# Kernel tuning notes

Hardware: AMD Instinct MI355X
Metric: run time of the kernel (lower is better)

Reference implementation:

```python
import jax, jax.numpy as jnp
import numpy as np

B, S, F, H = 256, 512, 64, 128


def setup_inputs() -> dict:
    key = jax.random.key(0)
    ks = jax.random.split(key, 16)
    u = lambda k, shape, fan: jax.random.uniform(k, shape, jnp.float32, -1.0 / np.sqrt(fan), 1.0 / np.sqrt(fan))
    inp = {
        'x': jax.random.normal(ks[0], (B, S, F), jnp.float32),
        'm': (jax.random.uniform(ks[1], (B, S, F)) < 0.8).astype(jnp.float32),
        't': jax.random.uniform(ks[2], (B, S, F), jnp.float32),
        # temp_decay_h: Linear(F -> H)
        'Wdh': u(ks[3], (H, F), H), 'bdh': u(ks[4], (H,), H),
        # temp_decay_m: diagonal Linear(F -> F)
        'Wdm': u(ks[5], (F, F), F), 'bdm': u(ks[6], (F,), F),
        # time_reg: Linear(H -> F)
        'Wtr': u(ks[7], (F, H), H), 'btr': u(ks[8], (F,), H),
        # feat_reg: masked Linear(F -> F), zero diagonal
        'Wfr': u(ks[9], (F, F), F), 'bfr': u(ks[10], (F,), F),
        # weight_combine: Linear(2F -> F)
        'Wwc': u(ks[11], (F, 2 * F), 2 * F), 'bwc': u(ks[12], (F,), 2 * F),
        # LSTMCell(2F -> H)
        'Wih': u(ks[13], (4 * H, 2 * F), H), 'Whh': u(ks[14], (4 * H, H), H),
        'bih': u(ks[15], (4 * H,), H), 'bhh': u(jax.random.fold_in(key, 99), (4 * H,), H),
    }
    return inp


def _rits_forward(x, m, t, Wdh, bdh, Wdm, bdm, Wtr, btr, Wfr, bfr, Wwc, bwc, Wih, Whh, bih, bhh):
    f = x.shape[-1]
    hdim = Whh.shape[1]
    dWdm = jnp.diagonal(Wdm)                 # diag-masked temporal decay weight
    Wfr_m = Wfr * (1.0 - jnp.eye(f, dtype=Wfr.dtype))

    def step(carry, inputs):
        h, c, loss = carry
        xl, ml, tl = inputs                  # [B,F] each
        gamma_h = jnp.exp(-jax.nn.relu(tl @ Wdh.T + bdh))   # [B,H]
        gamma_m = jnp.exp(-jax.nn.relu(tl * dWdm + bdm))    # [B,F]
        h = h * gamma_h
        xl_hat = h @ Wtr.T + btr             # history-based estimate [B,F]
        denom = jnp.sum(ml) + 1e-5
        loss = loss + jnp.sum((xl - xl_hat) ** 2 * ml) / denom
        xl_c = ml * xl + (1.0 - ml) * xl_hat
        zl_hat = xl_c @ Wfr_m.T + bfr        # feature-based estimate
        loss = loss + jnp.sum((xl - zl_hat) ** 2 * ml) / denom
        beta = jnp.concatenate([gamma_m, ml], axis=1) @ Wwc.T + bwc
        cl_hat = beta * zl_hat + (1.0 - beta) * xl_hat
        loss = loss + jnp.sum((xl - cl_hat) ** 2 * ml) / denom
        cl_c = ml * xl + (1.0 - ml) * cl_hat
        inp = jnp.concatenate([cl_c, ml], axis=1)           # [B,2F]
        gates = inp @ Wih.T + bih + h @ Whh.T + bhh         # [B,4H]
        i, fg, g, o = jnp.split(gates, 4, axis=1)
        i, fg, o = jax.nn.sigmoid(i), jax.nn.sigmoid(fg), jax.nn.sigmoid(o)
        c = fg * c + i * jnp.tanh(g)
        h = o * jnp.tanh(c)
        return (h, c, loss), cl_c

    b, s, _ = x.shape
    h0 = jnp.zeros((b, hdim), x.dtype)
    c0 = jnp.zeros((b, hdim), x.dtype)
    xs = (jnp.swapaxes(x, 0, 1), jnp.swapaxes(m, 0, 1), jnp.swapaxes(t, 0, 1))
    (h, c, loss), imps = jax.lax.scan(step, (h0, c0, jnp.float32(0.0)), xs)
    imputations = jnp.swapaxes(imps, 0, 1)   # [B,S,F]
    return imputations, loss / s


def reference(x, m, t, Wdh, bdh, Wdm, bdm, Wtr, btr, Wfr, bfr, Wwc, bwc, Wih, Whh, bih, bhh):
    return _rits_forward(x, m, t, Wdh, bdh, Wdm, bdm, Wtr, btr, Wfr, bfr, Wwc, bwc, Wih, Whh, bih, bhh)
```

## Files before the change

kernel.cpp:

```cpp
#include <hip/hip_runtime.h>
#include <hip/hip_bf16.h>

#define Bsz 256
#define Ssz 512
#define Fsz 64
#define Hsz 128
#define NG  512

typedef unsigned short ushort_t;
typedef __attribute__((ext_vector_type(8))) short short8v;
typedef __attribute__((ext_vector_type(4))) float float4v;

__device__ __forceinline__ ushort_t f2bf(float f) {
  unsigned int b = __float_as_uint(f);
  return (ushort_t)((b + 0x7fffu + ((b >> 16) & 1u)) >> 16);
}
__device__ __forceinline__ float bf2f(ushort_t u) {
  return __uint_as_float(((unsigned int)u) << 16);
}
__device__ __forceinline__ float sigf(float v) { return 1.f / (1.f + __expf(-v)); }
__device__ __forceinline__ float tanhf_fast(float v) {
  float e = __expf(2.f * v);
  return 1.f - 2.f / (e + 1.f);
}

__global__ void denom_kernel(const float* __restrict__ m, float* __restrict__ inv_denom) {
  int s = blockIdx.x;
  int tid = threadIdx.x;
  const float4* mp = (const float4*)(m + ((size_t)tid * Ssz + s) * Fsz);
  float sum = 0.f;
#pragma unroll
  for (int i = 0; i < Fsz / 4; ++i) {
    float4 v = mp[i];
    sum += v.x + v.y + v.z + v.w;
  }
  for (int off = 32; off > 0; off >>= 1) sum += __shfl_xor(sum, off);
  __shared__ float red[4];
  if ((tid & 63) == 0) red[tid >> 6] = sum;
  __syncthreads();
  if (tid == 0) {
    float tot = red[0] + red[1] + red[2] + red[3];
    inv_denom[s] = 1.0f / (tot + 1e-5f);
  }
}

__global__ void pack_kernel(const float* __restrict__ Wih, const float* __restrict__ Whh,
                            ushort_t* __restrict__ Wpk) {
  int g = blockIdx.x * blockDim.x + threadIdx.x;
  if (g >= 16384) return;
  int lane = g & 63, nt = (g >> 6) & 31, kt = g >> 11;
  int jout = nt * 16 + (lane & 15);
  int kbase = kt * 32 + ((lane >> 4) << 3);
  ushort_t* dst = Wpk + (size_t)g * 8;
#pragma unroll
  for (int j = 0; j < 8; ++j) {
    int k = kbase + j;
    float w = (k < 128) ? Wih[jout * 128 + k] : Whh[jout * 128 + (k - 128)];
    dst[j] = f2bf(w);
  }
}

__global__ void gh_kernel(const float* __restrict__ t, const float* __restrict__ Wdh,
                          const float* __restrict__ bdh, ushort_t* __restrict__ gh) {
  const int tid = threadIdx.x;
  const int lane = tid & 63, wv = tid >> 6;
  const int row0 = blockIdx.x * 64;
  __shared__ __align__(16) ushort_t st[64][72];
  __shared__ __align__(16) ushort_t sO[64][136];
  __shared__ float sbdh[128];
  if (tid < 128) sbdh[tid] = bdh[tid];
  short8v Bf[2][8];
#pragma unroll
  for (int kt = 0; kt < 2; ++kt)
#pragma unroll
    for (int nt = 0; nt < 8; ++nt) {
      int col = nt * 16 + (lane & 15);
      int k0 = kt * 32 + ((lane >> 4) << 3);
      float4 wa = *(const float4*)(Wdh + col * 64 + k0);
      float4 wb = *(const float4*)(Wdh + col * 64 + k0 + 4);
      short8v bb;
      bb[0] = (short)f2bf(wa.x); bb[1] = (short)f2bf(wa.y);
      bb[2] = (short)f2bf(wa.z); bb[3] = (short)f2bf(wa.w);
      bb[4] = (short)f2bf(wb.x); bb[5] = (short)f2bf(wb.y);
      bb[6] = (short)f2bf(wb.z); bb[7] = (short)f2bf(wb.w);
      Bf[kt][nt] = bb;
    }
  const float* tb = t + (size_t)row0 * 64;
  {
    int r = tid >> 2, c0 = (tid & 3) * 16;
#pragma unroll
    for (int q = 0; q < 4; ++q) {
      float4 v = *(const float4*)(tb + r * 64 + c0 + q * 4);
      st[r][c0 + q * 4 + 0] = f2bf(v.x);
      st[r][c0 + q * 4 + 1] = f2bf(v.y);
      st[r][c0 + q * 4 + 2] = f2bf(v.z);
      st[r][c0 + q * 4 + 3] = f2bf(v.w);
    }
  }
  __syncthreads();
  float4v acc[8] = {};
#pragma unroll
  for (int kt = 0; kt < 2; ++kt) {
    int r = wv * 16 + (lane & 15);
    int k0 = kt * 32 + ((lane >> 4) << 3);
    short8v a = *(const short8v*)&st[r][k0];
#pragma unroll
    for (int nt = 0; nt < 8; ++nt)
      acc[nt] = __builtin_amdgcn_mfma_f32_16x16x32_bf16(a, Bf[kt][nt], acc[nt], 0, 0, 0);
  }
#pragma unroll
  for (int nt = 0; nt < 8; ++nt)
#pragma unroll
    for (int rr = 0; rr < 4; ++rr) {
      int col = nt * 16 + (lane & 15);
      int row = wv * 16 + ((lane >> 4) << 2) + rr;
      float v = acc[nt][rr] + sbdh[col];
      sO[row][col] = f2bf(__expf(-fmaxf(0.f, v)));
    }
  __syncthreads();
  {
    int r = tid >> 2, c0 = (tid & 3) * 32;
    const uint4* src = (const uint4*)&sO[r][c0];
    uint4* dst = (uint4*)(gh + (size_t)(row0 + r) * 128 + c0);
#pragma unroll
    for (int q = 0; q < 4; ++q) dst[q] = src[q];
  }
}

__global__ void beta_kernel(const float* __restrict__ t, const float* __restrict__ m,
                            const float* __restrict__ Wdm, const float* __restrict__ bdm,
                            const float* __restrict__ Wwc, const float* __restrict__ bwc,
                            ushort_t* __restrict__ beta) {
  const int tid = threadIdx.x;
  const int lane = tid & 63, wv = tid >> 6;
  const int row0 = blockIdx.x * 64;
  __shared__ __align__(16) ushort_t sA[64][136];
  __shared__ __align__(16) ushort_t sO[64][72];
  __shared__ float sdw[64], sbd[64], sbwc[64];
  if (tid < 64) {
    sdw[tid] = Wdm[tid * 64 + tid];
    sbd[tid] = bdm[tid];
    sbwc[tid] = bwc[tid];
  }
  short8v Bf[4][4];
#pragma unroll
  for (int kt = 0; kt < 4; ++kt)
#pragma unroll
    for (int nt = 0; nt < 4; ++nt) {
      int col = nt * 16 + (lane & 15);
      int k0 = kt * 32 + ((lane >> 4) << 3);
      float4 wa = *(const float4*)(Wwc + col * 128 + k0);
      float4 wb = *(const float4*)(Wwc + col * 128 + k0 + 4);
      short8v bb;
      bb[0] = (short)f2bf(wa.x); bb[1] = (short)f2bf(wa.y);
      bb[2] = (short)f2bf(wa.z); bb[3] = (short)f2bf(wa.w);
      bb[4] = (short)f2bf(wb.x); bb[5] = (short)f2bf(wb.y);
      bb[6] = (short)f2bf(wb.z); bb[7] = (short)f2bf(wb.w);
      Bf[kt][nt] = bb;
    }
  __syncthreads();
  {
    int r = tid >> 2, c0 = (tid & 3) * 16;
    const float* tb = t + (size_t)row0 * 64;
    const float* mb = m + (size_t)row0 * 64;
#pragma unroll
    for (int q = 0; q < 4; ++q) {
      float4 tv = *(const float4*)(tb + r * 64 + c0 + q * 4);
      float4 mv = *(const float4*)(mb + r * 64 + c0 + q * 4);
      int c = c0 + q * 4;
      sA[r][c + 0] = f2bf(__expf(-fmaxf(0.f, tv.x * sdw[c + 0] + sbd[c + 0])));
      sA[r][c + 1] = f2bf(__expf(-fmaxf(0.f, tv.y * sdw[c + 1] + sbd[c + 1])));
      sA[r][c + 2] = f2bf(__expf(-fmaxf(0.f, tv.z * sdw[c + 2] + sbd[c + 2])));
      sA[r][c + 3] = f2bf(__expf(-fmaxf(0.f, tv.w * sdw[c + 3] + sbd[c + 3])));
      sA[r][64 + c + 0] = f2bf(mv.x);
      sA[r][64 + c + 1] = f2bf(mv.y);
      sA[r][64 + c + 2] = f2bf(mv.z);
      sA[r][64 + c + 3] = f2bf(mv.w);
    }
  }
  __syncthreads();
  float4v acc[4] = {};
#pragma unroll
  for (int kt = 0; kt < 4; ++kt) {
    int r = wv * 16 + (lane & 15);
    int k0 = kt * 32 + ((lane >> 4) << 3);
    short8v a = *(const short8v*)&sA[r][k0];
#pragma unroll
    for (int nt = 0; nt < 4; ++nt)
      acc[nt] = __builtin_amdgcn_mfma_f32_16x16x32_bf16(a, Bf[kt][nt], acc[nt], 0, 0, 0);
  }
#pragma unroll
  for (int nt = 0; nt < 4; ++nt)
#pragma unroll
    for (int rr = 0; rr < 4; ++rr) {
      int col = nt * 16 + (lane & 15);
      int row = wv * 16 + ((lane >> 4) << 2) + rr;
      sO[row][col] = f2bf(acc[nt][rr] + sbwc[col]);
    }
  __syncthreads();
  {
    int r = tid >> 2, c0 = (tid & 3) * 16;
    const uint4* src = (const uint4*)&sO[r][c0];
    uint4* dst = (uint4*)(beta + (size_t)(row0 + r) * 64 + c0);
    dst[0] = src[0];
    dst[1] = src[1];
  }
}

__launch_bounds__(512, 1)
__global__ void rits_kernel(
    const float* __restrict__ x, const float* __restrict__ m,
    const float* __restrict__ Wtr, const float* __restrict__ btr,
    const float* __restrict__ Wfr, const float* __restrict__ bfr,
    const float* __restrict__ bih, const float* __restrict__ bhh,
    const ushort_t* __restrict__ Wpk, const float* __restrict__ inv_denom,
    const ushort_t* __restrict__ ghp, const ushort_t* __restrict__ betap,
    float* __restrict__ out_imp, float* __restrict__ out_loss)
{
  const int b = blockIdx.x;
  const int tid = threadIdx.x;
  const int lane = tid & 63;
  const int wv = tid >> 6;

  __shared__ float sIdn[Ssz];
  __shared__ float sPart[8][64];
  __shared__ float sPartF[8][64];
  __shared__ float sGates[NG];
  __shared__ float sH[Hsz];
  __shared__ __align__(16) ushort_t sVh[256];

  sIdn[tid] = inv_denom[tid];

  float wtr_r[16];
  {
    const float* wb = Wtr + lane * 128 + wv * 16;
#pragma unroll
    for (int q = 0; q < 4; ++q) {
      float4 v = *(const float4*)(wb + q * 4);
      wtr_r[q * 4 + 0] = v.x; wtr_r[q * 4 + 1] = v.y;
      wtr_r[q * 4 + 2] = v.z; wtr_r[q * 4 + 3] = v.w;
    }
  }
  float wfr_r[8];
  {
    const float* wb = Wfr + lane * 64 + wv * 8;
#pragma unroll
    for (int q = 0; q < 2; ++q) {
      float4 v = *(const float4*)(wb + q * 4);
      wfr_r[q * 4 + 0] = v.x; wfr_r[q * 4 + 1] = v.y;
      wfr_r[q * 4 + 2] = v.z; wfr_r[q * 4 + 3] = v.w;
    }
#pragma unroll
    for (int i = 0; i < 8; ++i)
      if (lane == wv * 8 + i) wfr_r[i] = 0.f;
  }
  const float btr_r = btr[lane];
  const float bfr_r = bfr[lane];

  const short8v* wp = (const short8v*)Wpk;
  short8v Bf[8][4];
#pragma unroll
  for (int kt = 0; kt < 8; ++kt)
#pragma unroll
    for (int n = 0; n < 4; ++n)
      Bf[kt][n] = wp[((kt * 32 + wv * 4 + n) << 6) + lane];
  float gb[4];
#pragma unroll
  for (int n = 0; n < 4; ++n) {
    int j = (wv * 4 + n) * 16 + (lane & 15);
    gb[n] = bih[j] + bhh[j];
  }

  const float* xp = x + (size_t)b * Ssz * Fsz;
  const float* mp = m + (size_t)b * Ssz * Fsz;
  const ushort_t* ghb = ghp + (size_t)b * Ssz * 128;
  const ushort_t* beb = betap + (size_t)b * Ssz * 64;
  float* op = out_imp + (size_t)b * Ssz * Fsz;

  if (tid < Hsz) sH[tid] = 0.f;
  if (tid < 128) sVh[128 + tid] = 0;
  float c_reg = 0.f;

  float xv_cur = xp[lane];
  float mv_cur = mp[lane];
  float bet_cur = bf2f(beb[lane]);
  if (wv == 0) sVh[64 + lane] = f2bf(mv_cur);
  __syncthreads();

  float lacc = 0.f;

  for (int s = 0; s < Ssz; ++s) {
    const int ps = (s + 1 < Ssz) ? s + 1 : Ssz - 1;
    float xv_nxt = xp[ps * 64 + lane];
    float mv_nxt = mp[ps * 64 + lane];
    ushort_t bet_raw = beb[ps * 64 + lane];
    ushort_t gh_raw = 0;
    if (tid < 128) gh_raw = ghb[(size_t)ps * 128 + tid];

    {
      const float4* h4 = (const float4*)&sH[wv * 16];
      float4 h0 = h4[0], h1 = h4[1], h2 = h4[2], h3 = h4[3];
      float part = wtr_r[0] * h0.x + wtr_r[1] * h0.y + wtr_r[2] * h0.z + wtr_r[3] * h0.w
                 + wtr_r[4] * h1.x + wtr_r[5] * h1.y + wtr_r[6] * h1.z + wtr_r[7] * h1.w
                 + wtr_r[8] * h2.x + wtr_r[9] * h2.y + wtr_r[10] * h2.z + wtr_r[11] * h2.w
                 + wtr_r[12] * h3.x + wtr_r[13] * h3.y + wtr_r[14] * h3.z + wtr_r[15] * h3.w;
      sPart[wv][lane] = part;
    }

    float4v acc[4];
#pragma unroll
    for (int n = 0; n < 4; ++n) acc[n] = (float4v){gb[n], gb[n], gb[n], gb[n]};
    {
      const char* abase = (const char*)sVh + ((lane >> 4) << 4);
#pragma unroll
      for (int kt = 2; kt < 8; ++kt) {
        short8v a = *(const short8v*)(abase + kt * 64);
#pragma unroll
        for (int n = 0; n < 4; ++n)
          acc[n] = __builtin_amdgcn_mfma_f32_16x16x32_bf16(a, Bf[kt][n], acc[n], 0, 0, 0);
      }
    }
    __syncthreads();

    float xlh = btr_r;
#pragma unroll
    for (int w = 0; w < 8; ++w) xlh += sPart[w][lane];
    const float xv = xv_cur, mv = mv_cur;
    const float xlc = mv * xv + (1.f - mv) * xlh;
    const float idn = sIdn[s];
    if (wv == 0) { float d = xv - xlh; lacc += d * d * mv * idn; }
    {
      float pf = 0.f;
#pragma unroll
      for (int i = 0; i < 8; ++i) pf += wfr_r[i] * __shfl(xlc, wv * 8 + i);
      sPartF[wv][lane] = pf;
    }
    __syncthreads();

    float zl = bfr_r;
#pragma unroll
    for (int w = 0; w < 8; ++w) zl += sPartF[w][lane];
    const float beta = bet_cur;
    const float clh = beta * zl + (1.f - beta) * xlh;
    const float clc = mv * xv + (1.f - mv) * clh;
    if (wv == 0) {
      float d2 = xv - zl, d3 = xv - clh;
      lacc += (d2 * d2 + d3 * d3) * mv * idn;
      op[s * 64 + lane] = clc;
    }
    {
      const int kb = (lane >> 4) << 3;
      short8v A0, A1;
#pragma unroll
      for (int j = 0; j < 8; ++j) {
        A0[j] = (short)f2bf(__shfl(clc, kb + j));
        A1[j] = (short)f2bf(__shfl(clc, 32 + kb + j));
      }
#pragma unroll
      for (int n = 0; n < 4; ++n) {
        acc[n] = __builtin_amdgcn_mfma_f32_16x16x32_bf16(A0, Bf[0][n], acc[n], 0, 0, 0);
        acc[n] = __builtin_amdgcn_mfma_f32_16x16x32_bf16(A1, Bf[1][n], acc[n], 0, 0, 0);
      }
      if (lane < 16) {
#pragma unroll
        for (int n = 0; n < 4; ++n)
          sGates[(wv * 4 + n) * 16 + lane] = acc[n][0];
      }
    }
    __syncthreads();

    if (tid < 128) {
      float gi = sGates[tid], gf = sGates[128 + tid];
      float gg = sGates[256 + tid], go = sGates[384 + tid];
      float cc = sigf(gf) * c_reg + sigf(gi) * tanhf_fast(gg);
      c_reg = cc;
      float hn = sigf(go) * tanhf_fast(cc);
      float hv = hn * bf2f(gh_raw);
      sH[tid] = hv;
      sVh[128 + tid] = f2bf(hv);
    }
    if (wv == 0) sVh[64 + lane] = f2bf(mv_nxt);
    __syncthreads();

    xv_cur = xv_nxt;
    mv_cur = mv_nxt;
    bet_cur = bf2f(bet_raw);
  }

  if (wv == 0) {
    for (int off = 32; off > 0; off >>= 1) lacc += __shfl_xor(lacc, off);
    if (lane == 0) atomicAdd(out_loss, lacc * (1.0f / Ssz));
  }
}

extern "C" void kernel_launch(void* const* d_in, const int* in_sizes, int n_in,
                              void* d_out, int out_size, void* d_ws, size_t ws_size,
                              hipStream_t stream) {
  const float* x   = (const float*)d_in[0];
  const float* m   = (const float*)d_in[1];
  const float* t   = (const float*)d_in[2];
  const float* Wdh = (const float*)d_in[3];
  const float* bdh = (const float*)d_in[4];
  const float* Wdm = (const float*)d_in[5];
  const float* bdm = (const float*)d_in[6];
  const float* Wtr = (const float*)d_in[7];
  const float* btr = (const float*)d_in[8];
  const float* Wfr = (const float*)d_in[9];
  const float* bfr = (const float*)d_in[10];
  const float* Wwc = (const float*)d_in[11];
  const float* bwc = (const float*)d_in[12];
  const float* Wih = (const float*)d_in[13];
  const float* Whh = (const float*)d_in[14];
  const float* bih = (const float*)d_in[15];
  const float* bhh = (const float*)d_in[16];

  char* ws = (char*)d_ws;
  float* inv_denom = (float*)ws;
  ushort_t* Wpk    = (ushort_t*)(ws + 2048);
  ushort_t* gh_ws  = (ushort_t*)(ws + 264192);
  ushort_t* be_ws  = (ushort_t*)(ws + 264192 + (size_t)Bsz * Ssz * 128 * 2);
  float* out_f = (float*)d_out;
  float* out_loss = out_f + (size_t)Bsz * Ssz * Fsz;

  denom_kernel<<<Ssz, 256, 0, stream>>>(m, inv_denom);
  pack_kernel<<<64, 256, 0, stream>>>(Wih, Whh, Wpk);
  gh_kernel<<<(Bsz * Ssz) / 64, 256, 0, stream>>>(t, Wdh, bdh, gh_ws);
  beta_kernel<<<(Bsz * Ssz) / 64, 256, 0, stream>>>(t, m, Wdm, bdm, Wwc, bwc, be_ws);
  hipMemsetAsync(out_loss, 0, sizeof(float), stream);
  rits_kernel<<<Bsz, 512, 0, stream>>>(x, m, Wtr, btr, Wfr, bfr, bih, bhh,
                                       Wpk, inv_denom, gh_ws, be_ws, out_f, out_loss);
}
```

Baseline: 1.486 ms.

## Restructure RITS recurrence with MFMA regressions, gate-local LSTM, chunked staging

The history regression (Wtr) and feature regression (Wfr) move from per-lane fp32 dot products plus shared-memory partial reductions onto bf16 MFMA tiles held by a few waves. Gate columns are reassigned so each wave holds the i/f/g/o tiles for the same 16 hidden units, so the LSTM update runs in registers without a shared gates buffer. This cuts the per-step barriers from four to three. Per-step global loads of x, m, beta and gamma_h are replaced by 8-step double-buffered chunks staged into LDS. The regressions now take bf16 inputs, which loses precision, and the feature-regression stage runs on a single wave that sits on the critical path.

```diff
diff --git a/kernel.cpp b/kernel.cpp
--- a/kernel.cpp
+++ b/kernel.cpp
@@ -6,6 +6,7 @@
 #define Fsz 64
 #define Hsz 128
 #define NG  512
+#define CH  8
 
 typedef unsigned short ushort_t;
 typedef __attribute__((ext_vector_type(8))) short short8v;
@@ -22,6 +23,11 @@
 __device__ __forceinline__ float tanhf_fast(float v) {
   float e = __expf(2.f * v);
   return 1.f - 2.f / (e + 1.f);
+}
+__device__ __forceinline__ void bar_sync() {
+  asm volatile("s_waitcnt lgkmcnt(0)" ::: "memory");
+  __builtin_amdgcn_s_barrier();
+  asm volatile("" ::: "memory");
 }
 
 __global__ void denom_kernel(const float* __restrict__ m, float* __restrict__ inv_denom) {
@@ -221,41 +227,21 @@
   const int tid = threadIdx.x;
   const int lane = tid & 63;
   const int wv = tid >> 6;
+  const int l15 = lane & 15;
+  const int kg = lane >> 4;
 
   __shared__ float sIdn[Ssz];
-  __shared__ float sPart[8][64];
-  __shared__ float sPartF[8][64];
-  __shared__ float sGates[NG];
-  __shared__ float sH[Hsz];
-  __shared__ __align__(16) ushort_t sVh[256];
+  __shared__ __align__(16) ushort_t sHh[Hsz];
+  __shared__ __align__(16) ushort_t sXcF[Fsz];
+  __shared__ __align__(16) ushort_t sClcF[Fsz];
+  __shared__ float sXlhP[2][Fsz];
+  __shared__ __align__(16) float    sXb[2][CH][Fsz];
+  __shared__ __align__(16) ushort_t sMb[2][CH][Fsz];
+  __shared__ __align__(16) ushort_t sBb[2][CH][Fsz];
+  __shared__ __align__(16) ushort_t sGb[2][CH][Hsz];
 
   sIdn[tid] = inv_denom[tid];
-
-  float wtr_r[16];
-  {
-    const float* wb = Wtr + lane * 128 + wv * 16;
-#pragma unroll
-    for (int q = 0; q < 4; ++q) {
-      float4 v = *(const float4*)(wb + q * 4);
-      wtr_r[q * 4 + 0] = v.x; wtr_r[q * 4 + 1] = v.y;
-      wtr_r[q * 4 + 2] = v.z; wtr_r[q * 4 + 3] = v.w;
-    }
-  }
-  float wfr_r[8];
-  {
-    const float* wb = Wfr + lane * 64 + wv * 8;
-#pragma unroll
-    for (int q = 0; q < 2; ++q) {
-      float4 v = *(const float4*)(wb + q * 4);
-      wfr_r[q * 4 + 0] = v.x; wfr_r[q * 4 + 1] = v.y;
-      wfr_r[q * 4 + 2] = v.z; wfr_r[q * 4 + 3] = v.w;
-    }
-#pragma unroll
-    for (int i = 0; i < 8; ++i)
-      if (lane == wv * 8 + i) wfr_r[i] = 0.f;
-  }
-  const float btr_r = btr[lane];
-  const float bfr_r = bfr[lane];
+  if (tid < Hsz) sHh[tid] = 0;
 
   const short8v* wp = (const short8v*)Wpk;
   short8v Bf[8][4];
@@ -263,132 +249,210 @@
   for (int kt = 0; kt < 8; ++kt)
 #pragma unroll
     for (int n = 0; n < 4; ++n)
-      Bf[kt][n] = wp[((kt * 32 + wv * 4 + n) << 6) + lane];
+      Bf[kt][n] = wp[((kt * 32 + wv + 8 * n) << 6) + lane];
   float gb[4];
 #pragma unroll
   for (int n = 0; n < 4; ++n) {
-    int j = (wv * 4 + n) * 16 + (lane & 15);
+    int j = (wv + 8 * n) * 16 + l15;
     gb[n] = bih[j] + bhh[j];
+  }
+
+  short8v uW[8];
+  float btr_r[4] = {0.f, 0.f, 0.f, 0.f}, bfr_r[4] = {0.f, 0.f, 0.f, 0.f};
+  if (wv == 1 || wv == 3) {
+    const int ktb = (wv == 1) ? 0 : 2;
+#pragma unroll
+    for (int kt = 0; kt < 2; ++kt)
+#pragma unroll
+      for (int n = 0; n < 4; ++n) {
+        int col = n * 16 + l15;
+        int k0 = (ktb + kt) * 32 + kg * 8;
+        short8v bb;
+#pragma unroll
+        for (int j = 0; j < 8; ++j) bb[j] = (short)f2bf(Wtr[col * 128 + k0 + j]);
+        uW[kt * 4 + n] = bb;
+      }
+  } else if (wv == 2) {
+#pragma unroll
+    for (int kt = 0; kt < 2; ++kt)
+#pragma unroll
+      for (int n = 0; n < 4; ++n) {
+        int col = n * 16 + l15;
+        int k0 = kt * 32 + kg * 8;
+        short8v bb;
+#pragma unroll
+        for (int j = 0; j < 8; ++j) {
+          int k = k0 + j;
+          bb[j] = (k == col) ? (short)0 : (short)f2bf(Wfr[col * 64 + k]);
+        }
+        uW[kt * 4 + n] = bb;
+      }
+#pragma unroll
+    for (int n = 0; n < 4; ++n) {
+      btr_r[n] = btr[n * 16 + l15];
+      bfr_r[n] = bfr[n * 16 + l15];
+    }
   }
 
   const float* xp = x + (size_t)b * Ssz * Fsz;
   const float* mp = m + (size_t)b * Ssz * Fsz;
-  const ushort_t* ghb = ghp + (size_t)b * Ssz * 128;
-  const ushort_t* beb = betap + (size_t)b * Ssz * 64;
+  const ushort_t* ghb = ghp + (size_t)b * Ssz * Hsz;
+  const ushort_t* beb = betap + (size_t)b * Ssz * Fsz;
   float* op = out_imp + (size_t)b * Ssz * Fsz;
 
-  if (tid < Hsz) sH[tid] = 0.f;
-  if (tid < 128) sVh[128 + tid] = 0;
+  {
+    float x0 = xp[tid], m0 = mp[tid];
+    ushort_t b0 = beb[tid];
+    int st0 = 1 + (tid >> 7);
+    int st1 = st0 + 4;
+    ushort_t g0 = ghb[(size_t)st0 * Hsz + (tid & 127)];
+    ushort_t g1 = ghb[(size_t)st1 * Hsz + (tid & 127)];
+    sXb[0][tid >> 6][tid & 63] = x0;
+    sMb[0][tid >> 6][tid & 63] = f2bf(m0);
+    sBb[0][tid >> 6][tid & 63] = b0;
+    sGb[0][tid >> 7][tid & 127] = g0;
+    sGb[0][4 + (tid >> 7)][tid & 127] = g1;
+  }
+  __syncthreads();
+
+  float lacc = 0.f;
   float c_reg = 0.f;
-
-  float xv_cur = xp[lane];
-  float mv_cur = mp[lane];
-  float bet_cur = bf2f(beb[lane]);
-  if (wv == 0) sVh[64 + lane] = f2bf(mv_cur);
-  __syncthreads();
-
-  float lacc = 0.f;
+  float x_r = 0.f, m_r = 0.f;
+  ushort_t be_r = 0, gh_r0 = 0, gh_r1 = 0;
 
   for (int s = 0; s < Ssz; ++s) {
-    const int ps = (s + 1 < Ssz) ? s + 1 : Ssz - 1;
-    float xv_nxt = xp[ps * 64 + lane];
-    float mv_nxt = mp[ps * 64 + lane];
-    ushort_t bet_raw = beb[ps * 64 + lane];
-    ushort_t gh_raw = 0;
-    if (tid < 128) gh_raw = ghb[(size_t)ps * 128 + tid];
-
-    {
-      const float4* h4 = (const float4*)&sH[wv * 16];
-      float4 h0 = h4[0], h1 = h4[1], h2 = h4[2], h3 = h4[3];
-      float part = wtr_r[0] * h0.x + wtr_r[1] * h0.y + wtr_r[2] * h0.z + wtr_r[3] * h0.w
-                 + wtr_r[4] * h1.x + wtr_r[5] * h1.y + wtr_r[6] * h1.z + wtr_r[7] * h1.w
-                 + wtr_r[8] * h2.x + wtr_r[9] * h2.y + wtr_r[10] * h2.z + wtr_r[11] * h2.w
-                 + wtr_r[12] * h3.x + wtr_r[13] * h3.y + wtr_r[14] * h3.z + wtr_r[15] * h3.w;
-      sPart[wv][lane] = part;
-    }
+    const int p = (s >> 3) & 1, sc = s & 7;
+
+    if (sc == 0 && s + CH < Ssz) {
+      int base = (s + CH) * Fsz;
+      x_r = xp[base + tid];
+      m_r = mp[base + tid];
+      be_r = beb[base + tid];
+      int st0 = s + CH + 1 + (tid >> 7);
+      int st1 = st0 + 4;
+      if (st0 > Ssz - 1) st0 = Ssz - 1;
+      if (st1 > Ssz - 1) st1 = Ssz - 1;
+      gh_r0 = ghb[(size_t)st0 * Hsz + (tid & 127)];
+      gh_r1 = ghb[(size_t)st1 * Hsz + (tid & 127)];
+    }
+    const char* hbase = (const char*)sHh + kg * 16;
+    short8v ah0 = *(const short8v*)(hbase);
+    short8v ah1 = *(const short8v*)(hbase + 64);
+    short8v ah2 = *(const short8v*)(hbase + 128);
+    short8v ah3 = *(const short8v*)(hbase + 192);
+    const char* mbase = (const char*)sMb[p][sc] + kg * 16;
+    short8v am0 = *(const short8v*)(mbase);
+    short8v am1 = *(const short8v*)(mbase + 64);
 
     float4v acc[4];
 #pragma unroll
     for (int n = 0; n < 4; ++n) acc[n] = (float4v){gb[n], gb[n], gb[n], gb[n]};
-    {
-      const char* abase = (const char*)sVh + ((lane >> 4) << 4);
-#pragma unroll
-      for (int kt = 2; kt < 8; ++kt) {
-        short8v a = *(const short8v*)(abase + kt * 64);
-#pragma unroll
-        for (int n = 0; n < 4; ++n)
-          acc[n] = __builtin_amdgcn_mfma_f32_16x16x32_bf16(a, Bf[kt][n], acc[n], 0, 0, 0);
-      }
-    }
-    __syncthreads();
-
-    float xlh = btr_r;
-#pragma unroll
-    for (int w = 0; w < 8; ++w) xlh += sPart[w][lane];
-    const float xv = xv_cur, mv = mv_cur;
-    const float xlc = mv * xv + (1.f - mv) * xlh;
-    const float idn = sIdn[s];
-    if (wv == 0) { float d = xv - xlh; lacc += d * d * mv * idn; }
-    {
-      float pf = 0.f;
-#pragma unroll
-      for (int i = 0; i < 8; ++i) pf += wfr_r[i] * __shfl(xlc, wv * 8 + i);
-      sPartF[wv][lane] = pf;
-    }
-    __syncthreads();
-
-    float zl = bfr_r;
-#pragma unroll
-    for (int w = 0; w < 8; ++w) zl += sPartF[w][lane];
-    const float beta = bet_cur;
-    const float clh = beta * zl + (1.f - beta) * xlh;
-    const float clc = mv * xv + (1.f - mv) * clh;
-    if (wv == 0) {
-      float d2 = xv - zl, d3 = xv - clh;
-      lacc += (d2 * d2 + d3 * d3) * mv * idn;
-      op[s * 64 + lane] = clc;
-    }
-    {
-      const int kb = (lane >> 4) << 3;
-      short8v A0, A1;
-#pragma unroll
-      for (int j = 0; j < 8; ++j) {
-        A0[j] = (short)f2bf(__shfl(clc, kb + j));
-        A1[j] = (short)f2bf(__shfl(clc, 32 + kb + j));
-      }
+#pragma unroll
+    for (int n = 0; n < 4; ++n) {
+      acc[n] = __builtin_amdgcn_mfma_f32_16x16x32_bf16(am0, Bf[2][n], acc[n], 0, 0, 0);
+      acc[n] = __builtin_amdgcn_mfma_f32_16x16x32_bf16(am1, Bf[3][n], acc[n], 0, 0, 0);
+      acc[n] = __builtin_amdgcn_mfma_f32_16x16x32_bf16(ah0, Bf[4][n], acc[n], 0, 0, 0);
+      acc[n] = __builtin_amdgcn_mfma_f32_16x16x32_bf16(ah1, Bf[5][n], acc[n], 0, 0, 0);
+      acc[n] = __builtin_amdgcn_mfma_f32_16x16x32_bf16(ah2, Bf[6][n], acc[n], 0, 0, 0);
+      acc[n] = __builtin_amdgcn_mfma_f32_16x16x32_bf16(ah3, Bf[7][n], acc[n], 0, 0, 0);
+    }
+    if (wv == 1 || wv == 3) {
+      short8v a0 = (wv == 1) ? ah0 : ah2;
+      short8v a1 = (wv == 1) ? ah1 : ah3;
+      float4v xacc[4];
+#pragma unroll
+      for (int n = 0; n < 4; ++n) xacc[n] = (float4v){0.f, 0.f, 0.f, 0.f};
 #pragma unroll
       for (int n = 0; n < 4; ++n) {
-        acc[n] = __builtin_amdgcn_mfma_f32_16x16x32_bf16(A0, Bf[0][n], acc[n], 0, 0, 0);
-        acc[n] = __builtin_amdgcn_mfma_f32_16x16x32_bf16(A1, Bf[1][n], acc[n], 0, 0, 0);
+        xacc[n] = __builtin_amdgcn_mfma_f32_16x16x32_bf16(a0, uW[n], xacc[n], 0, 0, 0);
+        xacc[n] = __builtin_amdgcn_mfma_f32_16x16x32_bf16(a1, uW[4 + n], xacc[n], 0, 0, 0);
       }
       if (lane < 16) {
-#pragma unroll
-        for (int n = 0; n < 4; ++n)
-          sGates[(wv * 4 + n) * 16 + lane] = acc[n][0];
-      }
-    }
-    __syncthreads();
-
-    if (tid < 128) {
-      float gi = sGates[tid], gf = sGates[128 + tid];
-      float gg = sGates[256 + tid], go = sGates[384 + tid];
-      float cc = sigf(gf) * c_reg + sigf(gi) * tanhf_fast(gg);
+        const int w = (wv == 1) ? 0 : 1;
+#pragma unroll
+        for (int n = 0; n < 4; ++n) sXlhP[w][n * 16 + lane] = xacc[n][0];
+      }
+    }
+    bar_sync();
+
+    if (wv == 2) {
+      const float idn = sIdn[s];
+      float xlh[4], xv[4], mv[4], bev[4], xlc[4];
+#pragma unroll
+      for (int n = 0; n < 4; ++n) {
+        int f = n * 16 + l15;
+        xlh[n] = sXlhP[0][f] + sXlhP[1][f] + btr_r[n];
+        xv[n] = sXb[p][sc][f];
+        mv[n] = bf2f(sMb[p][sc][f]);
+        bev[n] = bf2f(sBb[p][sc][f]);
+        xlc[n] = mv[n] * xv[n] + (1.f - mv[n]) * xlh[n];
+      }
+      if (lane < 16) {
+#pragma unroll
+        for (int n = 0; n < 4; ++n) {
+          float d = xv[n] - xlh[n];
+          lacc += d * d * mv[n] * idn;
+          sXcF[n * 16 + lane] = f2bf(xlc[n]);
+        }
+      }
+      const char* xbase = (const char*)sXcF + kg * 16;
+      short8v ax0 = *(const short8v*)(xbase);
+      short8v ax1 = *(const short8v*)(xbase + 64);
+      float4v zac[4];
+#pragma unroll
+      for (int n = 0; n < 4; ++n) zac[n] = (float4v){0.f, 0.f, 0.f, 0.f};
+#pragma unroll
+      for (int n = 0; n < 4; ++n) {
+        zac[n] = __builtin_amdgcn_mfma_f32_16x16x32_bf16(ax0, uW[n], zac[n], 0, 0, 0);
+        zac[n] = __builtin_amdgcn_mfma_f32_16x16x32_bf16(ax1, uW[4 + n], zac[n], 0, 0, 0);
+      }
+      if (lane < 16) {
+#pragma unroll
+        for (int n = 0; n < 4; ++n) {
+          float zl = zac[n][0] + bfr_r[n];
+          float clh = bev[n] * zl + (1.f - bev[n]) * xlh[n];
+          float d2 = xv[n] - zl, d3 = xv[n] - clh;
+          lacc += (d2 * d2 + d3 * d3) * mv[n] * idn;
+          float clc = mv[n] * xv[n] + (1.f - mv[n]) * clh;
+          sClcF[n * 16 + lane] = f2bf(clc);
+          op[s * Fsz + n * 16 + lane] = clc;
+        }
+      }
+    }
+    bar_sync();
+
+    const char* cbase = (const char*)sClcF + kg * 16;
+    short8v ac0 = *(const short8v*)(cbase);
+    short8v ac1 = *(const short8v*)(cbase + 64);
+#pragma unroll
+    for (int n = 0; n < 4; ++n) {
+      acc[n] = __builtin_amdgcn_mfma_f32_16x16x32_bf16(ac0, Bf[0][n], acc[n], 0, 0, 0);
+      acc[n] = __builtin_amdgcn_mfma_f32_16x16x32_bf16(ac1, Bf[1][n], acc[n], 0, 0, 0);
+    }
+    if (lane < 16) {
+      const int hh = wv * 16 + lane;
+      float cc = sigf(acc[1][0]) * c_reg + sigf(acc[0][0]) * tanhf_fast(acc[2][0]);
       c_reg = cc;
-      float hn = sigf(go) * tanhf_fast(cc);
-      float hv = hn * bf2f(gh_raw);
-      sH[tid] = hv;
-      sVh[128 + tid] = f2bf(hv);
-    }
-    if (wv == 0) sVh[64 + lane] = f2bf(mv_nxt);
-    __syncthreads();
-
-    xv_cur = xv_nxt;
-    mv_cur = mv_nxt;
-    bet_cur = bf2f(bet_raw);
-  }
-
-  if (wv == 0) {
-    for (int off = 32; off > 0; off >>= 1) lacc += __shfl_xor(lacc, off);
+      float hn = sigf(acc[3][0]) * tanhf_fast(cc);
+      float hv = hn * bf2f(sGb[p][sc][hh]);
+      sHh[hh] = f2bf(hv);
+    }
+    if (sc == 7 && s + 1 < Ssz) {
+      const int q = p ^ 1;
+      sXb[q][tid >> 6][tid & 63] = x_r;
+      sMb[q][tid >> 6][tid & 63] = f2bf(m_r);
+      sBb[q][tid >> 6][tid & 63] = be_r;
+      sGb[q][tid >> 7][tid & 127] = gh_r0;
+      sGb[q][4 + (tid >> 7)][tid & 127] = gh_r1;
+    }
+    bar_sync();
+  }
+
+  if (wv == 2 && lane < 16) {
+    lacc += __shfl_xor(lacc, 1);
+    lacc += __shfl_xor(lacc, 2);
+    lacc += __shfl_xor(lacc, 4);
+    lacc += __shfl_xor(lacc, 8);
     if (lane == 0) atomicAdd(out_loss, lacc * (1.0f / Ssz));
   }
 }
```

Measured after the change: 1.598 ms. +7.6%, slower.

## Batch 16 sequences per block and run the recurrence on MFMA tiles

Applied to the files above, without the earlier changes.

Each block now processes 16 batch rows at once, so the MFMA M dimension is filled with real rows instead of one, and the grid shrinks from 256 to 16 blocks. The history and feature regressions move from scalar dot products plus shared-memory reductions onto bf16 MFMA. Inputs are prefetched in double-buffered chunks of 4 timesteps, and the steps are split across wave halves so gate work overlaps the regression work. The cost is only 16 of the GPU's CUs in use, bf16 rounding of Wtr, Wfr and the hidden state, and a larger shared-memory footprint.

```diff
diff --git a/kernel.cpp b/kernel.cpp
--- a/kernel.cpp
+++ b/kernel.cpp
@@ -6,6 +6,8 @@
 #define Fsz 64
 #define Hsz 128
 #define NG  512
+#define GR  16
+#define CH  4
 
 typedef unsigned short ushort_t;
 typedef __attribute__((ext_vector_type(8))) short short8v;
@@ -22,6 +24,11 @@
 __device__ __forceinline__ float tanhf_fast(float v) {
   float e = __expf(2.f * v);
   return 1.f - 2.f / (e + 1.f);
+}
+__device__ __forceinline__ void bar_sync() {
+  asm volatile("s_waitcnt lgkmcnt(0)" ::: "memory");
+  __builtin_amdgcn_s_barrier();
+  asm volatile("" ::: "memory");
 }
 
 __global__ void denom_kernel(const float* __restrict__ m, float* __restrict__ inv_denom) {
@@ -217,45 +224,22 @@
     const ushort_t* __restrict__ ghp, const ushort_t* __restrict__ betap,
     float* __restrict__ out_imp, float* __restrict__ out_loss)
 {
-  const int b = blockIdx.x;
+  const int b0 = blockIdx.x * GR;
   const int tid = threadIdx.x;
   const int lane = tid & 63;
   const int wv = tid >> 6;
+  const int l15 = lane & 15;
+  const int kg = lane >> 4;
 
   __shared__ float sIdn[Ssz];
-  __shared__ float sPart[8][64];
-  __shared__ float sPartF[8][64];
-  __shared__ float sGates[NG];
-  __shared__ float sH[Hsz];
-  __shared__ __align__(16) ushort_t sVh[256];
-
-  sIdn[tid] = inv_denom[tid];
-
-  float wtr_r[16];
-  {
-    const float* wb = Wtr + lane * 128 + wv * 16;
-#pragma unroll
-    for (int q = 0; q < 4; ++q) {
-      float4 v = *(const float4*)(wb + q * 4);
-      wtr_r[q * 4 + 0] = v.x; wtr_r[q * 4 + 1] = v.y;
-      wtr_r[q * 4 + 2] = v.z; wtr_r[q * 4 + 3] = v.w;
-    }
-  }
-  float wfr_r[8];
-  {
-    const float* wb = Wfr + lane * 64 + wv * 8;
-#pragma unroll
-    for (int q = 0; q < 2; ++q) {
-      float4 v = *(const float4*)(wb + q * 4);
-      wfr_r[q * 4 + 0] = v.x; wfr_r[q * 4 + 1] = v.y;
-      wfr_r[q * 4 + 2] = v.z; wfr_r[q * 4 + 3] = v.w;
-    }
-#pragma unroll
-    for (int i = 0; i < 8; ++i)
-      if (lane == wv * 8 + i) wfr_r[i] = 0.f;
-  }
-  const float btr_r = btr[lane];
-  const float bfr_r = bfr[lane];
+  __shared__ __align__(16) ushort_t sV[GR][264];
+  __shared__ __align__(16) float    sXlh[GR][68];
+  __shared__ __align__(16) ushort_t sXcF[GR][72];
+  __shared__ __align__(16) float    sXb[2][CH][GR][68];
+  __shared__ __align__(16) ushort_t sMb[2][CH][GR][72];
+  __shared__ __align__(16) ushort_t sBb[2][CH][GR][72];
+  __shared__ __align__(16) ushort_t sGb[2][CH][GR][136];
+  __shared__ float sRed[8];
 
   const short8v* wp = (const short8v*)Wpk;
   short8v Bf[8][4];
@@ -263,133 +247,233 @@
   for (int kt = 0; kt < 8; ++kt)
 #pragma unroll
     for (int n = 0; n < 4; ++n)
-      Bf[kt][n] = wp[((kt * 32 + wv * 4 + n) << 6) + lane];
+      Bf[kt][n] = wp[((kt * 32 + wv + 8 * n) << 6) + lane];
   float gb[4];
 #pragma unroll
   for (int n = 0; n < 4; ++n) {
-    int j = (wv * 4 + n) * 16 + (lane & 15);
+    int j = (wv + 8 * n) * 16 + l15;
     gb[n] = bih[j] + bhh[j];
   }
 
-  const float* xp = x + (size_t)b * Ssz * Fsz;
-  const float* mp = m + (size_t)b * Ssz * Fsz;
-  const ushort_t* ghb = ghp + (size_t)b * Ssz * 128;
-  const ushort_t* beb = betap + (size_t)b * Ssz * 64;
-  float* op = out_imp + (size_t)b * Ssz * Fsz;
-
-  if (tid < Hsz) sH[tid] = 0.f;
-  if (tid < 128) sVh[128 + tid] = 0;
-  float c_reg = 0.f;
-
-  float xv_cur = xp[lane];
-  float mv_cur = mp[lane];
-  float bet_cur = bf2f(beb[lane]);
-  if (wv == 0) sVh[64 + lane] = f2bf(mv_cur);
+  short8v uW[4];
+  float btr_r = 0.f, bfr_r = 0.f;
+  if (wv < 4) {
+    const int col = wv * 16 + l15;
+#pragma unroll
+    for (int kt = 0; kt < 4; ++kt) {
+      int k0 = kt * 32 + kg * 8;
+      short8v bb;
+#pragma unroll
+      for (int j = 0; j < 8; ++j) bb[j] = (short)f2bf(Wtr[col * 128 + k0 + j]);
+      uW[kt] = bb;
+    }
+    btr_r = btr[col];
+  } else {
+    const int col = (wv - 4) * 16 + l15;
+#pragma unroll
+    for (int kt = 0; kt < 2; ++kt) {
+      int k0 = kt * 32 + kg * 8;
+      short8v bb;
+#pragma unroll
+      for (int j = 0; j < 8; ++j) {
+        int k = k0 + j;
+        bb[j] = (k == col) ? (short)0 : (short)f2bf(Wfr[col * 64 + k]);
+      }
+      uW[kt] = bb;
+    }
+    uW[2] = uW[0]; uW[3] = uW[1];
+    bfr_r = bfr[col];
+  }
+
+  const int sg2 = tid >> 7;
+  const int rg  = (tid >> 3) & 15;
+  const int fg8 = (tid & 7) * 8;
+  const int hg16 = (tid & 7) * 16;
+  const float*    xbase = x     + (size_t)(b0 + rg) * Ssz * Fsz + sg2 * 64 + fg8;
+  const float*    mbase = m     + (size_t)(b0 + rg) * Ssz * Fsz + sg2 * 64 + fg8;
+  const ushort_t* bbase = betap + (size_t)(b0 + rg) * Ssz * Fsz + sg2 * 64 + fg8;
+  const size_t    ghoff = (size_t)(b0 + rg) * Ssz * Hsz + hg16;
+  float* op = out_imp + (size_t)b0 * Ssz * Fsz;
+
+  {
+    float4 a = *(const float4*)xbase, b2 = *(const float4*)(xbase + 4);
+    *(float4*)&sXb[0][sg2][rg][fg8]     = a;
+    *(float4*)&sXb[0][sg2][rg][fg8 + 4] = b2;
+    float4 ma = *(const float4*)mbase, mb2 = *(const float4*)(mbase + 4);
+    uint4 mq;
+    mq.x = (unsigned)f2bf(ma.x)  | ((unsigned)f2bf(ma.y)  << 16);
+    mq.y = (unsigned)f2bf(ma.z)  | ((unsigned)f2bf(ma.w)  << 16);
+    mq.z = (unsigned)f2bf(mb2.x) | ((unsigned)f2bf(mb2.y) << 16);
+    mq.w = (unsigned)f2bf(mb2.z) | ((unsigned)f2bf(mb2.w) << 16);
+    *(uint4*)&sMb[0][sg2][rg][fg8] = mq;
+    if (sg2 == 0) *(uint4*)&sV[rg][64 + fg8] = mq;
+    *(uint4*)&sBb[0][sg2][rg][fg8] = *(const uint4*)bbase;
+    const ushort_t* gp_ = ghp + ghoff + (size_t)(sg2 + 1) * 128;
+    *(uint4*)&sGb[0][sg2][rg][hg16]     = *(const uint4*)gp_;
+    *(uint4*)&sGb[0][sg2][rg][hg16 + 8] = *(const uint4*)(gp_ + 8);
+    *(unsigned long long*)&sV[tid >> 5][128 + (tid & 31) * 4] = 0ULL;
+    sIdn[tid] = inv_denom[tid];
+  }
   __syncthreads();
 
   float lacc = 0.f;
-
+  float c_reg[4] = {0.f, 0.f, 0.f, 0.f};
+  float4 xr0, xr1, mr0, mr1;
+  uint4 ber, gr0, gr1;
+
+  const char* vrow = (const char*)sV + l15 * 528 + kg * 16;
+
+#pragma unroll 4
   for (int s = 0; s < Ssz; ++s) {
-    const int ps = (s + 1 < Ssz) ? s + 1 : Ssz - 1;
-    float xv_nxt = xp[ps * 64 + lane];
-    float mv_nxt = mp[ps * 64 + lane];
-    ushort_t bet_raw = beb[ps * 64 + lane];
-    ushort_t gh_raw = 0;
-    if (tid < 128) gh_raw = ghb[(size_t)ps * 128 + tid];
-
-    {
-      const float4* h4 = (const float4*)&sH[wv * 16];
-      float4 h0 = h4[0], h1 = h4[1], h2 = h4[2], h3 = h4[3];
-      float part = wtr_r[0] * h0.x + wtr_r[1] * h0.y + wtr_r[2] * h0.z + wtr_r[3] * h0.w
-                 + wtr_r[4] * h1.x + wtr_r[5] * h1.y + wtr_r[6] * h1.z + wtr_r[7] * h1.w
-                 + wtr_r[8] * h2.x + wtr_r[9] * h2.y + wtr_r[10] * h2.z + wtr_r[11] * h2.w
-                 + wtr_r[12] * h3.x + wtr_r[13] * h3.y + wtr_r[14] * h3.z + wtr_r[15] * h3.w;
-      sPart[wv][lane] = part;
-    }
+    const int p = (s >> 2) & 1, sc = s & 3;
+    const float idn = sIdn[s];
+
+    if (sc == 0 && s + CH < Ssz) {
+      const int cs = s + CH;
+      xr0 = *(const float4*)(xbase + cs * 64);
+      xr1 = *(const float4*)(xbase + cs * 64 + 4);
+      mr0 = *(const float4*)(mbase + cs * 64);
+      mr1 = *(const float4*)(mbase + cs * 64 + 4);
+      ber = *(const uint4*)(bbase + cs * 64);
+      int st = cs + sg2 + 1; if (st > Ssz - 1) st = Ssz - 1;
+      const ushort_t* gp_ = ghp + ghoff + (size_t)st * 128;
+      gr0 = *(const uint4*)gp_;
+      gr1 = *(const uint4*)(gp_ + 8);
+    }
+
+    short8v ah0 = *(const short8v*)(vrow + 256);
+    short8v ah1 = *(const short8v*)(vrow + 320);
+    short8v ah2 = *(const short8v*)(vrow + 384);
+    short8v ah3 = *(const short8v*)(vrow + 448);
 
     float4v acc[4];
 #pragma unroll
     for (int n = 0; n < 4; ++n) acc[n] = (float4v){gb[n], gb[n], gb[n], gb[n]};
-    {
-      const char* abase = (const char*)sVh + ((lane >> 4) << 4);
-#pragma unroll
-      for (int kt = 2; kt < 8; ++kt) {
-        short8v a = *(const short8v*)(abase + kt * 64);
-#pragma unroll
-        for (int n = 0; n < 4; ++n)
-          acc[n] = __builtin_amdgcn_mfma_f32_16x16x32_bf16(a, Bf[kt][n], acc[n], 0, 0, 0);
-      }
-    }
-    __syncthreads();
-
-    float xlh = btr_r;
-#pragma unroll
-    for (int w = 0; w < 8; ++w) xlh += sPart[w][lane];
-    const float xv = xv_cur, mv = mv_cur;
-    const float xlc = mv * xv + (1.f - mv) * xlh;
-    const float idn = sIdn[s];
-    if (wv == 0) { float d = xv - xlh; lacc += d * d * mv * idn; }
-    {
-      float pf = 0.f;
-#pragma unroll
-      for (int i = 0; i < 8; ++i) pf += wfr_r[i] * __shfl(xlc, wv * 8 + i);
-      sPartF[wv][lane] = pf;
-    }
-    __syncthreads();
-
-    float zl = bfr_r;
-#pragma unroll
-    for (int w = 0; w < 8; ++w) zl += sPartF[w][lane];
-    const float beta = bet_cur;
-    const float clh = beta * zl + (1.f - beta) * xlh;
-    const float clc = mv * xv + (1.f - mv) * clh;
-    if (wv == 0) {
-      float d2 = xv - zl, d3 = xv - clh;
-      lacc += (d2 * d2 + d3 * d3) * mv * idn;
-      op[s * 64 + lane] = clc;
-    }
-    {
-      const int kb = (lane >> 4) << 3;
-      short8v A0, A1;
-#pragma unroll
-      for (int j = 0; j < 8; ++j) {
-        A0[j] = (short)f2bf(__shfl(clc, kb + j));
-        A1[j] = (short)f2bf(__shfl(clc, 32 + kb + j));
-      }
+
+    if (wv < 4) {
 #pragma unroll
       for (int n = 0; n < 4; ++n) {
-        acc[n] = __builtin_amdgcn_mfma_f32_16x16x32_bf16(A0, Bf[0][n], acc[n], 0, 0, 0);
-        acc[n] = __builtin_amdgcn_mfma_f32_16x16x32_bf16(A1, Bf[1][n], acc[n], 0, 0, 0);
-      }
-      if (lane < 16) {
-#pragma unroll
-        for (int n = 0; n < 4; ++n)
-          sGates[(wv * 4 + n) * 16 + lane] = acc[n][0];
-      }
-    }
-    __syncthreads();
-
-    if (tid < 128) {
-      float gi = sGates[tid], gf = sGates[128 + tid];
-      float gg = sGates[256 + tid], go = sGates[384 + tid];
-      float cc = sigf(gf) * c_reg + sigf(gi) * tanhf_fast(gg);
-      c_reg = cc;
-      float hn = sigf(go) * tanhf_fast(cc);
-      float hv = hn * bf2f(gh_raw);
-      sH[tid] = hv;
-      sVh[128 + tid] = f2bf(hv);
-    }
-    if (wv == 0) sVh[64 + lane] = f2bf(mv_nxt);
-    __syncthreads();
-
-    xv_cur = xv_nxt;
-    mv_cur = mv_nxt;
-    bet_cur = bf2f(bet_raw);
-  }
-
-  if (wv == 0) {
-    for (int off = 32; off > 0; off >>= 1) lacc += __shfl_xor(lacc, off);
-    if (lane == 0) atomicAdd(out_loss, lacc * (1.0f / Ssz));
+        acc[n] = __builtin_amdgcn_mfma_f32_16x16x32_bf16(ah0, Bf[4][n], acc[n], 0, 0, 0);
+        acc[n] = __builtin_amdgcn_mfma_f32_16x16x32_bf16(ah1, Bf[5][n], acc[n], 0, 0, 0);
+      }
+      float4v xacc = (float4v){0.f, 0.f, 0.f, 0.f};
+      xacc = __builtin_amdgcn_mfma_f32_16x16x32_bf16(ah0, uW[0], xacc, 0, 0, 0);
+      xacc = __builtin_amdgcn_mfma_f32_16x16x32_bf16(ah1, uW[1], xacc, 0, 0, 0);
+      xacc = __builtin_amdgcn_mfma_f32_16x16x32_bf16(ah2, uW[2], xacc, 0, 0, 0);
+      xacc = __builtin_amdgcn_mfma_f32_16x16x32_bf16(ah3, uW[3], xacc, 0, 0, 0);
+      const int fc = wv * 16 + l15;
+#pragma unroll
+      for (int r = 0; r < 4; ++r) {
+        const int row = kg * 4 + r;
+        float xl = xacc[r] + btr_r;
+        float xv = sXb[p][sc][row][fc];
+        float mv = bf2f(sMb[p][sc][row][fc]);
+        float xlc = mv * xv + (1.f - mv) * xl;
+        float d = xv - xl;
+        lacc += d * d * mv * idn;
+        sXlh[row][fc] = xl;
+        sXcF[row][fc] = f2bf(xlc);
+      }
+    } else {
+      short8v am0 = *(const short8v*)(vrow + 128);
+      short8v am1 = *(const short8v*)(vrow + 192);
+#pragma unroll
+      for (int n = 0; n < 4; ++n) {
+        acc[n] = __builtin_amdgcn_mfma_f32_16x16x32_bf16(am0, Bf[2][n], acc[n], 0, 0, 0);
+        acc[n] = __builtin_amdgcn_mfma_f32_16x16x32_bf16(am1, Bf[3][n], acc[n], 0, 0, 0);
+        acc[n] = __builtin_amdgcn_mfma_f32_16x16x32_bf16(ah0, Bf[4][n], acc[n], 0, 0, 0);
+        acc[n] = __builtin_amdgcn_mfma_f32_16x16x32_bf16(ah1, Bf[5][n], acc[n], 0, 0, 0);
+        acc[n] = __builtin_amdgcn_mfma_f32_16x16x32_bf16(ah2, Bf[6][n], acc[n], 0, 0, 0);
+        acc[n] = __builtin_amdgcn_mfma_f32_16x16x32_bf16(ah3, Bf[7][n], acc[n], 0, 0, 0);
+      }
+    }
+    bar_sync();
+
+    if (wv < 4) {
+      short8v am0 = *(const short8v*)(vrow + 128);
+      short8v am1 = *(const short8v*)(vrow + 192);
+#pragma unroll
+      for (int n = 0; n < 4; ++n) {
+        acc[n] = __builtin_amdgcn_mfma_f32_16x16x32_bf16(am0, Bf[2][n], acc[n], 0, 0, 0);
+        acc[n] = __builtin_amdgcn_mfma_f32_16x16x32_bf16(am1, Bf[3][n], acc[n], 0, 0, 0);
+        acc[n] = __builtin_amdgcn_mfma_f32_16x16x32_bf16(ah2, Bf[6][n], acc[n], 0, 0, 0);
+        acc[n] = __builtin_amdgcn_mfma_f32_16x16x32_bf16(ah3, Bf[7][n], acc[n], 0, 0, 0);
+      }
+    } else {
+      const char* xrow = (const char*)sXcF + l15 * 144 + kg * 16;
+      short8v ax0 = *(const short8v*)(xrow);
+      short8v ax1 = *(const short8v*)(xrow + 64);
+      float4v zacc = (float4v){0.f, 0.f, 0.f, 0.f};
+      zacc = __builtin_amdgcn_mfma_f32_16x16x32_bf16(ax0, uW[0], zacc, 0, 0, 0);
+      zacc = __builtin_amdgcn_mfma_f32_16x16x32_bf16(ax1, uW[1], zacc, 0, 0, 0);
+      const int fc = (wv - 4) * 16 + l15;
+#pragma unroll
+      for (int r = 0; r < 4; ++r) {
+        const int row = kg * 4 + r;
+        float zl = zacc[r] + bfr_r;
+        float xlh = sXlh[row][fc];
+        float bev = bf2f(sBb[p][sc][row][fc]);
+        float xv = sXb[p][sc][row][fc];
+        float mv = bf2f(sMb[p][sc][row][fc]);
+        float clh = bev * zl + (1.f - bev) * xlh;
+        float d2 = xv - zl, d3 = xv - clh;
+        lacc += (d2 * d2 + d3 * d3) * mv * idn;
+        float clc = mv * xv + (1.f - mv) * clh;
+        sV[row][fc] = f2bf(clc);
+        op[(size_t)row * Ssz * Fsz + s * 64 + fc] = clc;
+      }
+    }
+    bar_sync();
+
+    short8v ac0 = *(const short8v*)(vrow);
+    short8v ac1 = *(const short8v*)(vrow + 64);
+#pragma unroll
+    for (int n = 0; n < 4; ++n) {
+      acc[n] = __builtin_amdgcn_mfma_f32_16x16x32_bf16(ac0, Bf[0][n], acc[n], 0, 0, 0);
+      acc[n] = __builtin_amdgcn_mfma_f32_16x16x32_bf16(ac1, Bf[1][n], acc[n], 0, 0, 0);
+    }
+    const int hidx = wv * 16 + l15;
+#pragma unroll
+    for (int r = 0; r < 4; ++r) {
+      const int row = kg * 4 + r;
+      float cc = sigf(acc[1][r]) * c_reg[r] + sigf(acc[0][r]) * tanhf_fast(acc[2][r]);
+      c_reg[r] = cc;
+      float hn = sigf(acc[3][r]) * tanhf_fast(cc);
+      float hv = hn * bf2f(sGb[p][sc][row][hidx]);
+      sV[row][128 + hidx] = f2bf(hv);
+    }
+    if (sc == 3) {
+      if (s + 1 < Ssz) {
+        const int q = p ^ 1;
+        uint4 mq;
+        mq.x = (unsigned)f2bf(mr0.x) | ((unsigned)f2bf(mr0.y) << 16);
+        mq.y = (unsigned)f2bf(mr0.z) | ((unsigned)f2bf(mr0.w) << 16);
+        mq.z = (unsigned)f2bf(mr1.x) | ((unsigned)f2bf(mr1.y) << 16);
+        mq.w = (unsigned)f2bf(mr1.z) | ((unsigned)f2bf(mr1.w) << 16);
+        *(float4*)&sXb[q][sg2][rg][fg8]     = xr0;
+        *(float4*)&sXb[q][sg2][rg][fg8 + 4] = xr1;
+        *(uint4*)&sMb[q][sg2][rg][fg8] = mq;
+        *(uint4*)&sBb[q][sg2][rg][fg8] = ber;
+        *(uint4*)&sGb[q][sg2][rg][hg16]     = gr0;
+        *(uint4*)&sGb[q][sg2][rg][hg16 + 8] = gr1;
+        if (sg2 == 0) *(uint4*)&sV[rg][64 + fg8] = mq;
+      }
+    } else {
+      const int row = tid >> 5, c2 = (tid & 31) * 2;
+      unsigned int mm = *(const unsigned int*)&sMb[p][sc + 1][row][c2];
+      *(unsigned int*)&sV[row][64 + c2] = mm;
+    }
+    bar_sync();
+  }
+
+  for (int off = 32; off > 0; off >>= 1) lacc += __shfl_xor(lacc, off);
+  if (lane == 0) sRed[wv] = lacc;
+  __syncthreads();
+  if (tid == 0) {
+    float tot = 0.f;
+#pragma unroll
+    for (int w = 0; w < 8; ++w) tot += sRed[w];
+    atomicAdd(out_loss, tot * (1.0f / Ssz));
   }
 }
 
@@ -427,6 +511,6 @@
   gh_kernel<<<(Bsz * Ssz) / 64, 256, 0, stream>>>(t, Wdh, bdh, gh_ws);
   beta_kernel<<<(Bsz * Ssz) / 64, 256, 0, stream>>>(t, m, Wdm, bdm, Wwc, bwc, be_ws);
   hipMemsetAsync(out_loss, 0, sizeof(float), stream);
-  rits_kernel<<<Bsz, 512, 0, stream>>>(x, m, Wtr, btr, Wfr, bfr, bih, bhh,
-                                       Wpk, inv_denom, gh_ws, be_ws, out_f, out_loss);
-}
+  rits_kernel<<<Bsz / GR, 512, 0, stream>>>(x, m, Wtr, btr, Wfr, bfr, bih, bhh,
+                                            Wpk, inv_denom, gh_ws, be_ws, out_f, out_loss);
+}
```

Measured after the change: 1.893 ms. 1.27x slower.
